# Kernel tuning notes

Measured on AMD Instinct MI355X. Metric: run time of the kernel, lower is better.

## Reference

```python
import jax, jax.numpy as jnp
import numpy as np

# config (matches init_kwargs)
NA, NEN = 8, 8            # n_agents, n_enemies
NENT = NA + NEN           # n_entities
NFA, NFE = 64, 64         # state_nf_al, state_nf_en
E, A, M, HE = 64, 64, 32, 64  # entity_embed, attn_embed, mixing_embed, hypernet_embed
TD, TE = 64, 64           # task_repre_dim, task_repre_embed_dim
BS, SL = 64, 512


def setup_inputs() -> dict:
    key = jax.random.key(0)
    ks = iter(jax.random.split(key, 32))
    def rn(shape, scale=0.05):
        return jax.random.normal(next(ks), shape, dtype=jnp.float32) * scale
    return {
        "agent_qs": rn((BS, SL, NA), 1.0),
        "states": rn((BS, SL, NA * NFA + NEN * NFE), 1.0),
        "task_repre_mu": rn((BS, SL, NA, TD), 1.0),
        "ally_w": rn((NFA, E)), "ally_b": rn((E,)),
        "enemy_w": rn((NFE, E)), "enemy_b": rn((E,)),
        "q_w": rn((E, A)), "q_b": rn((A,)),
        "k_w": rn((E, A)), "k_b": rn((A,)),
        "hw1_w1": rn((E + NFA + TE, HE)), "hw1_b1": rn((HE,)),
        "hw1_w2": rn((HE, M)), "hw1_b2": rn((M,)),
        "hwf_w1": rn((E + TE, HE)), "hwf_b1": rn((HE,)),
        "hwf_w2": rn((HE, M)), "hwf_b2": rn((M,)),
        "hb1_w": rn((E + TE, M)), "hb1_b": rn((M,)),
        "v_w1": rn((E + TE, M)), "v_b1": rn((M,)),
        "v_w2": rn((M, 1)), "v_b2": rn((1,)),
        "tre_w": rn((TD, TE)), "tre_b": rn((TE,)),
    }


def reference(agent_qs, states, task_repre_mu,
              ally_w, ally_b, enemy_w, enemy_b,
              q_w, q_b, k_w, k_b,
              hw1_w1, hw1_b1, hw1_w2, hw1_b2,
              hwf_w1, hwf_b1, hwf_w2, hwf_b2,
              hb1_w, hb1_b, v_w1, v_b1, v_w2, v_b2,
              tre_w, tre_b):
    bs, sl = agent_qs.shape[:2]
    # decompose_state (state_last_action=False, state_timestep_number=False)
    ally = states[..., : NA * NFA].reshape(bs, sl, NA, NFA)      # [bs,sl,NA,NFA]
    enemy = states[..., NA * NFA:].reshape(bs, sl, NEN, NFE)     # [bs,sl,NEN,NFE]
    ally_e = ally @ ally_w + ally_b                              # [bs,sl,NA,E]
    enemy_e = enemy @ enemy_w + enemy_b                          # [bs,sl,NEN,E]
    ent = jnp.concatenate([ally_e, enemy_e], axis=2)             # [bs,sl,NENT,E]
    q = ent @ q_w + q_b                                          # [bs,sl,NENT,A]
    k = ent @ k_w + k_b
    energy = jnp.einsum('bsqa,bska->bsqk', q, k)                 # [bs,sl,NENT,NENT]
    # torch: F.softmax(energy, dim=1) on [B,n_ent,n_ent] -> softmax over query axis
    attn = jax.nn.softmax(energy, axis=2)
    # attn_out = bmm(value[B,E,n], attn[B,n,n]).mean(-1)
    attn_out = jnp.einsum('bsne,bsnk->bse', ent, attn) / NENT    # [bs,sl,E]

    mean_mu = task_repre_mu.mean(axis=-2)                        # [bs,sl,TD]
    tre = task_repre_mu @ tre_w + tre_b                          # [bs,sl,NA,TE]
    mean_tre = mean_mu @ tre_w + tre_b                           # [bs,sl,TE]

    ent_mix = jnp.concatenate([
        jnp.broadcast_to(attn_out[:, :, None, :], (bs, sl, NA, E)),
        ally, tre], axis=-1)                                     # [bs,sl,NA,E+NFA+TE]
    mix = jnp.concatenate([attn_out, mean_tre], axis=-1)         # [bs,sl,E+TE]

    w1 = jnp.abs(jax.nn.relu(ent_mix @ hw1_w1 + hw1_b1) @ hw1_w2 + hw1_b2)  # [bs,sl,NA,M]
    b1 = mix @ hb1_w + hb1_b                                     # [bs,sl,M]
    hidden = jax.nn.elu(jnp.einsum('bsn,bsnm->bsm', agent_qs, w1) + b1)     # [bs,sl,M]
    wf = jnp.abs(jax.nn.relu(mix @ hwf_w1 + hwf_b1) @ hwf_w2 + hwf_b2)      # [bs,sl,M]
    v = jax.nn.relu(mix @ v_w1 + v_b1) @ v_w2 + v_b2             # [bs,sl,1]
    q_tot = jnp.einsum('bsm,bsm->bs', hidden, wf)[..., None] + v # [bs,sl,1]
    return q_tot
```

## Files before the change

### kernel.cpp

```cpp
#include <hip/hip_runtime.h>
#include <math.h>


#define TOKS 32768

typedef __attribute__((ext_vector_type(8))) short short8;
typedef __attribute__((ext_vector_type(4))) float f32x4;

#define MFMA(a, b, c) __builtin_amdgcn_mfma_f32_16x16x32_bf16((a), (b), (c), 0, 0, 0)

#define E_CAT   0
#define E_WQKT  8192
#define E_ZBRT  13312
#define E_H1T   29696
#define E_W2T   41984
#define E_WFT   44032
#define E_BF16_TOTAL 46080
#define E_AO_US 46464

__device__ __forceinline__ unsigned short bfr(float x) {
    unsigned u = __builtin_bit_cast(unsigned, x);
    u += 0x7fffu + ((u >> 16) & 1u);
    return (unsigned short)(u >> 16);
}
__device__ __forceinline__ float bf2f(unsigned short h) {
    unsigned u = ((unsigned)h) << 16;
    return __builtin_bit_cast(float, u);
}
__device__ __forceinline__ short8 cvt8v(float4 a, float4 b) {
    short8 r;
    r[0] = (short)bfr(a.x); r[1] = (short)bfr(a.y);
    r[2] = (short)bfr(a.z); r[3] = (short)bfr(a.w);
    r[4] = (short)bfr(b.x); r[5] = (short)bfr(b.y);
    r[6] = (short)bfr(b.z); r[7] = (short)bfr(b.w);
    return r;
}
#define SWZ64(r, c)  ((((r) * 64)  + (c)) ^ (((r) & 7) << 3))
#define SWZ128(r, c) ((((r) * 128) + (c)) ^ (((r) & 7) << 3))
#define SWZ192(r, c) ((((r) * 192) + (c)) ^ (((r) & 7) << 3))

__global__ __launch_bounds__(256) void qmix_setup(
    const float* __restrict__ ally_w, const float* __restrict__ enemy_w,
    const float* __restrict__ q_w, const float* __restrict__ k_w,
    const float* __restrict__ k_b,
    const float* __restrict__ hw1_w1, const float* __restrict__ hw1_b1,
    const float* __restrict__ hw1_w2,
    const float* __restrict__ hwf_w1, const float* __restrict__ hwf_b1,
    const float* __restrict__ hwf_w2,
    const float* __restrict__ hb1_w, const float* __restrict__ hb1_b,
    const float* __restrict__ v_w1, const float* __restrict__ v_b1,
    const float* __restrict__ tre_w, const float* __restrict__ tre_b,
    unsigned short* __restrict__ wsb, float* __restrict__ wsf)
{
    int gid = blockIdx.x * 256 + threadIdx.x;
    if (gid < E_BF16_TOTAL) {
        float v = 0.f;
        int base, r, c, K;
        if (gid < E_WQKT) {
            base = E_CAT; K = 128;
            int i = gid - base; r = i >> 7; c = i & 127;
            v = (c < 64) ? ally_w[c * 64 + r] : enemy_w[(c - 64) * 64 + r];
        } else if (gid < E_ZBRT) {
            base = E_WQKT; K = 64;
            int i = gid - base; r = i >> 6; c = i & 63;
            if (r < 64) {
                for (int g = 0; g < 64; ++g) v += q_w[c * 64 + g] * k_w[r * 64 + g];
            } else if (r == 64) {
                for (int g = 0; g < 64; ++g) v += q_w[c * 64 + g] * k_b[g];
            }
        } else if (gid < E_H1T) {
            base = E_ZBRT; K = 128;
            int i = gid - base; r = i >> 7; c = i & 127;
            if (r < 64) {
                if (c < 64) v = hwf_w1[c * 64 + r];
                else for (int g = 0; g < 64; ++g) v += tre_w[(c - 64) * 64 + g] * hwf_w1[(64 + g) * 64 + r];
            } else if (r < 96) {
                int m = r - 64;
                if (c < 64) v = hb1_w[c * 32 + m];
                else for (int g = 0; g < 64; ++g) v += tre_w[(c - 64) * 64 + g] * hb1_w[(64 + g) * 32 + m];
            } else {
                int m = r - 96;
                if (c < 64) v = v_w1[c * 32 + m];
                else for (int g = 0; g < 64; ++g) v += tre_w[(c - 64) * 64 + g] * v_w1[(64 + g) * 32 + m];
            }
        } else if (gid < E_W2T) {
            base = E_H1T; K = 192;
            int i = gid - base; r = i / 192; c = i % 192;
            if (c < 64) v = hw1_w1[(64 + c) * 64 + r];
            else if (c < 128) {
                for (int g = 0; g < 64; ++g) v += tre_w[(c - 64) * 64 + g] * hw1_w1[(128 + g) * 64 + r];
            } else v = hw1_w1[(c - 128) * 64 + r];
        } else if (gid < E_WFT) {
            base = E_W2T; K = 64;
            int i = gid - base; r = i >> 6; c = i & 63;
            v = hw1_w2[c * 32 + r];
        } else {
            base = E_WFT; K = 64;
            int i = gid - base; r = i >> 6; c = i & 63;
            v = hwf_w2[c * 32 + r];
        }
        wsb[base + ((r * K + c) ^ ((r & 7) << 3))] = bfr(v);
    } else if (gid < E_BF16_TOTAL + 192) {
        int j = gid - E_BF16_TOTAL; float v;
        if (j < 64) {
            v = hw1_b1[j];
            for (int g = 0; g < 64; ++g) v += tre_b[g] * hw1_w1[(128 + g) * 64 + j];
        } else if (j < 128) {
            int e = j - 64; v = hwf_b1[e];
            for (int g = 0; g < 64; ++g) v += tre_b[g] * hwf_w1[(64 + g) * 64 + e];
        } else if (j < 160) {
            int m = j - 128; v = hb1_b[m];
            for (int g = 0; g < 64; ++g) v += tre_b[g] * hb1_w[(64 + g) * 32 + m];
        } else {
            int m = j - 160; v = v_b1[m];
            for (int g = 0; g < 64; ++g) v += tre_b[g] * v_w1[(64 + g) * 32 + m];
        }
        wsf[j] = v;
    }
}

__global__ __launch_bounds__(512) void qmix_attn(
    const float* __restrict__ states,
    const float* __restrict__ ally_b, const float* __restrict__ enemy_b,
    const unsigned short* __restrict__ wsb,
    unsigned short* __restrict__ aoG)
{
    __shared__ unsigned short sWa[13312];
    __shared__ unsigned short sE[8][1024];
    __shared__ unsigned short sT[8][1024];

    const int lane = threadIdx.x & 63;
    const int wv   = threadIdx.x >> 6;
    const int l15  = lane & 15;
    const int lg   = lane >> 4;
    const int kb   = lg * 8;
    const int tok0 = blockIdx.x * 32;

    const short8 zero8 = {0, 0, 0, 0, 0, 0, 0, 0};
    const f32x4  zero4 = {0.f, 0.f, 0.f, 0.f};

    for (int i = threadIdx.x * 8; i < 13312; i += 512 * 8)
        *(short8*)(sWa + i) = *(const short8*)(wsb + E_CAT + i);
    __syncthreads();
    const unsigned short* lCAT  = sWa;
    const unsigned short* lWQKT = sWa + 8192;

    unsigned short* E = sE[wv];
    unsigned short* T = sT[wv];

    float biasEnt[4];
    #pragma unroll
    for (int nt = 0; nt < 4; ++nt) {
        int col = nt * 16 + l15;
        biasEnt[nt] = (lg < 2) ? ally_b[col] : enemy_b[col];
    }

    const int roff = (l15 < 8) ? (l15 * 64 + kb) : (512 + (l15 - 8) * 64 + kb);
    float4 pf[4];
    {
        const float* p = states + (size_t)(tok0 + wv * 4) * 1024 + roff;
        pf[0] = *(const float4*)(p);      pf[1] = *(const float4*)(p + 4);
        pf[2] = *(const float4*)(p + 32); pf[3] = *(const float4*)(p + 36);
    }

    for (int ti = 0; ti < 4; ++ti) {
        const size_t t = (size_t)(tok0 + wv * 4 + ti);
        float4 cur0 = pf[0], cur1 = pf[1], cur2 = pf[2], cur3 = pf[3];
        if (ti < 3) {
            const float* p = states + (t + 1) * 1024 + roff;
            pf[0] = *(const float4*)(p);      pf[1] = *(const float4*)(p + 4);
            pf[2] = *(const float4*)(p + 32); pf[3] = *(const float4*)(p + 36);
        }
        short8 a01 = cvt8v(cur0, cur1);
        short8 a23 = cvt8v(cur2, cur3);
        const bool isally = (l15 < 8);

        f32x4 accB[4] = {zero4, zero4, zero4, zero4};
        #pragma unroll
        for (int ks = 0; ks < 4; ++ks) {
            short8 af;
            if (ks == 0)      af = isally ? a01 : zero8;
            else if (ks == 1) af = isally ? a23 : zero8;
            else if (ks == 2) af = isally ? zero8 : a01;
            else              af = isally ? zero8 : a23;
            #pragma unroll
            for (int nt = 0; nt < 4; ++nt) {
                short8 w = *(const short8*)&lCAT[SWZ128(nt * 16 + l15, ks * 32 + kb)];
                accB[nt] = MFMA(af, w, accB[nt]);
            }
        }
        float entv[4][4];
        #pragma unroll
        for (int nt = 0; nt < 4; ++nt) {
            #pragma unroll
            for (int reg = 0; reg < 4; ++reg) {
                entv[nt][reg] = accB[nt][reg] + biasEnt[nt];
                E[SWZ64(lg * 4 + reg, nt * 16 + l15)] = bfr(entv[nt][reg]);
            }
        }

        f32x4 accC[5] = {zero4, zero4, zero4, zero4, zero4};
        #pragma unroll
        for (int ks = 0; ks < 2; ++ks) {
            short8 ef = *(const short8*)&E[SWZ64(l15, ks * 32 + kb)];
            #pragma unroll
            for (int nt = 0; nt < 5; ++nt) {
                short8 w = *(const short8*)&lWQKT[SWZ64(nt * 16 + l15, ks * 32 + kb)];
                accC[nt] = MFMA(ef, w, accC[nt]);
            }
        }
        const int src = lane & 48;
        float si[4];
        #pragma unroll
        for (int reg = 0; reg < 4; ++reg) si[reg] = __shfl(accC[4][reg], src);
        #pragma unroll
        for (int nt = 0; nt < 4; ++nt)
            #pragma unroll
            for (int reg = 0; reg < 4; ++reg)
                T[SWZ64(lg * 4 + reg, nt * 16 + l15)] = bfr(accC[nt][reg]);

        f32x4 en = zero4;
        #pragma unroll
        for (int ks = 0; ks < 2; ++ks) {
            short8 ta = *(const short8*)&T[SWZ64(l15, ks * 32 + kb)];
            short8 ba = *(const short8*)&E[SWZ64(l15, ks * 32 + kb)];
            en = MFMA(ta, ba, en);
        }
        #pragma unroll
        for (int reg = 0; reg < 4; ++reg) en[reg] += si[reg];

        float mx = fmaxf(fmaxf(en[0], en[1]), fmaxf(en[2], en[3]));
        mx = fmaxf(mx, __shfl_xor(mx, 16));
        mx = fmaxf(mx, __shfl_xor(mx, 32));
        float p0 = __expf(en[0] - mx), p1 = __expf(en[1] - mx);
        float p2 = __expf(en[2] - mx), p3 = __expf(en[3] - mx);
        float s = p0 + p1 + p2 + p3;
        s += __shfl_xor(s, 16);
        s += __shfl_xor(s, 32);
        float inv = 1.f / s;
        float r0 = p0 * inv, r1 = p1 * inv, r2 = p2 * inv, r3 = p3 * inv;
        r0 += __shfl_xor(r0, 1); r0 += __shfl_xor(r0, 2); r0 += __shfl_xor(r0, 4); r0 += __shfl_xor(r0, 8);
        r1 += __shfl_xor(r1, 1); r1 += __shfl_xor(r1, 2); r1 += __shfl_xor(r1, 4); r1 += __shfl_xor(r1, 8);
        r2 += __shfl_xor(r2, 1); r2 += __shfl_xor(r2, 2); r2 += __shfl_xor(r2, 4); r2 += __shfl_xor(r2, 8);
        r3 += __shfl_xor(r3, 1); r3 += __shfl_xor(r3, 2); r3 += __shfl_xor(r3, 4); r3 += __shfl_xor(r3, 8);

        float part[4];
        #pragma unroll
        for (int nt = 0; nt < 4; ++nt) {
            float pp = r0 * entv[nt][0] + r1 * entv[nt][1]
                     + r2 * entv[nt][2] + r3 * entv[nt][3];
            pp += __shfl_xor(pp, 16);
            pp += __shfl_xor(pp, 32);
            part[nt] = pp;
        }
        float ao = (lg == 0) ? part[0] : (lg == 1) ? part[1]
                 : (lg == 2) ? part[2] : part[3];
        aoG[t * 64 + lane] = bfr(ao * 0.0625f);
    }
}

__device__ __forceinline__ short8 mmfrag(const float* __restrict__ mp) {
    float a0 = 0.f, a1 = 0.f, a2 = 0.f, a3 = 0.f, a4 = 0.f, a5 = 0.f, a6 = 0.f, a7 = 0.f;
    #pragma unroll
    for (int a = 0; a < 8; ++a) {
        float4 u = *(const float4*)(mp + a * 64);
        float4 v = *(const float4*)(mp + a * 64 + 4);
        a0 += u.x; a1 += u.y; a2 += u.z; a3 += u.w;
        a4 += v.x; a5 += v.y; a6 += v.z; a7 += v.w;
    }
    return cvt8v(make_float4(a0 * 0.125f, a1 * 0.125f, a2 * 0.125f, a3 * 0.125f),
                 make_float4(a4 * 0.125f, a5 * 0.125f, a6 * 0.125f, a7 * 0.125f));
}

__global__ __launch_bounds__(256) void qmix_hyper(
    const float* __restrict__ agent_qs, const float* __restrict__ states,
    const float* __restrict__ mu,
    const float* __restrict__ v_w2, const float* __restrict__ v_b2,
    const float* __restrict__ hw1_b2, const float* __restrict__ hwf_b2,
    const unsigned short* __restrict__ wsb, const float* __restrict__ wsf,
    const unsigned short* __restrict__ aoG,
    float* __restrict__ out)
{
    __shared__ unsigned short sWb[16384];
    __shared__ unsigned short sZ[4][1024];
    __shared__ unsigned short sH1[4][2048];
    __shared__ float sB1[4][512];
    __shared__ float sWF[4][512];
    __shared__ float sV[4][16];

    const int lane = threadIdx.x & 63;
    const int wv   = threadIdx.x >> 6;
    const int l15  = lane & 15;
    const int lg   = lane >> 4;
    const int kb   = lg * 8;
    const int T0   = blockIdx.x * 64 + wv * 16;

    const float* BHF = wsf + 64;
    const float* BB1 = wsf + 128;
    const float* BV  = wsf + 160;
    const float* BH1 = wsf + 0;

    const f32x4 zero4 = {0.f, 0.f, 0.f, 0.f};

    for (int i = threadIdx.x * 8; i < 16384; i += 256 * 8)
        *(short8*)(sWb + i) = *(const short8*)(wsb + E_ZBRT + i);
    __syncthreads();

    f32x4 zb[8] = {zero4, zero4, zero4, zero4, zero4, zero4, zero4, zero4};
    #pragma unroll
    for (int ks = 0; ks < 4; ++ks) {
        short8 af;
        if (ks < 2)
            af = *(const short8*)&aoG[(size_t)(T0 + l15) * 64 + ks * 32 + kb];
        else
            af = mmfrag(mu + (size_t)(T0 + l15) * 512 + (ks - 2) * 32 + kb);
        #pragma unroll
        for (int nt = 0; nt < 8; ++nt) {
            short8 w = *(const short8*)&sWb[SWZ128(nt * 16 + l15, ks * 32 + kb)];
            zb[nt] = MFMA(af, w, zb[nt]);
        }
    }
    __syncthreads();

    for (int i = threadIdx.x * 8; i < 16384; i += 256 * 8)
        *(short8*)(sWb + i) = *(const short8*)(wsb + E_H1T + i);

    #pragma unroll
    for (int nt = 0; nt < 4; ++nt) {
        int col = nt * 16 + l15;
        float bz = BHF[col];
        #pragma unroll
        for (int reg = 0; reg < 4; ++reg)
            sZ[wv][SWZ64(lg * 4 + reg, col)] = bfr(fmaxf(zb[nt][reg] + bz, 0.f));
    }
    #pragma unroll
    for (int nt = 4; nt < 6; ++nt) {
        int m = (nt - 4) * 16 + l15;
        float bb = BB1[m];
        #pragma unroll
        for (int reg = 0; reg < 4; ++reg)
            sB1[wv][(lg * 4 + reg) * 32 + m] = zb[nt][reg] + bb;
    }
    {
        float bv0 = BV[l15], bv1 = BV[16 + l15];
        float vw0 = v_w2[l15], vw1 = v_w2[16 + l15];
        #pragma unroll
        for (int reg = 0; reg < 4; ++reg) {
            float vp = fmaxf(zb[6][reg] + bv0, 0.f) * vw0
                     + fmaxf(zb[7][reg] + bv1, 0.f) * vw1;
            vp += __shfl_xor(vp, 1); vp += __shfl_xor(vp, 2);
            vp += __shfl_xor(vp, 4); vp += __shfl_xor(vp, 8);
            if (l15 == 0) sV[wv][lg * 4 + reg] = vp;
        }
    }
    __syncthreads();
    const unsigned short* lH1T = sWb;
    const unsigned short* lW2T = sWb + 12288;
    const unsigned short* lWFT = sWb + 14336;

    {
        f32x4 wfa = zero4, wfb = zero4;
        #pragma unroll
        for (int ks = 0; ks < 2; ++ks) {
            short8 af = *(const short8*)&sZ[wv][SWZ64(l15, ks * 32 + kb)];
            short8 b0 = *(const short8*)&lWFT[SWZ64(l15, ks * 32 + kb)];
            short8 b1 = *(const short8*)&lWFT[SWZ64(16 + l15, ks * 32 + kb)];
            wfa = MFMA(af, b0, wfa);
            wfb = MFMA(af, b1, wfb);
        }
        float hb0 = hwf_b2[l15], hb1 = hwf_b2[16 + l15];
        #pragma unroll
        for (int reg = 0; reg < 4; ++reg) {
            int tok = lg * 4 + reg;
            sWF[wv][tok * 32 + l15]      = fabsf(wfa[reg] + hb0);
            sWF[wv][tok * 32 + 16 + l15] = fabsf(wfb[reg] + hb1);
        }
    }

    const float vb2 = v_b2[0];
    const float b20 = hw1_b2[l15], b21 = hw1_b2[16 + l15];
    const int agent = l15 & 7;

    for (int c = 0; c < 4; ++c) {
        f32x4 h[2][4] = {{zero4, zero4, zero4, zero4}, {zero4, zero4, zero4, zero4}};
        #pragma unroll
        for (int ks = 0; ks < 6; ++ks) {
            #pragma unroll
            for (int ff = 0; ff < 2; ++ff) {
                const size_t tok = (size_t)(T0 + c * 4 + ff * 2 + (l15 >> 3));
                short8 af;
                if (ks < 2)
                    af = cvt8v(*(const float4*)(states + tok * 1024 + agent * 64 + ks * 32 + kb),
                               *(const float4*)(states + tok * 1024 + agent * 64 + ks * 32 + kb + 4));
                else if (ks < 4)
                    af = cvt8v(*(const float4*)(mu + tok * 512 + agent * 64 + (ks - 2) * 32 + kb),
                               *(const float4*)(mu + tok * 512 + agent * 64 + (ks - 2) * 32 + kb + 4));
                else
                    af = *(const short8*)&aoG[tok * 64 + (ks - 4) * 32 + kb];
                #pragma unroll
                for (int nt = 0; nt < 4; ++nt) {
                    short8 w = *(const short8*)&lH1T[SWZ192(nt * 16 + l15, ks * 32 + kb)];
                    h[ff][nt] = MFMA(af, w, h[ff][nt]);
                }
            }
        }
        #pragma unroll
        for (int ff = 0; ff < 2; ++ff)
            #pragma unroll
            for (int nt = 0; nt < 4; ++nt) {
                int col = nt * 16 + l15;
                float bh = BH1[col];
                #pragma unroll
                for (int reg = 0; reg < 4; ++reg)
                    sH1[wv][SWZ64(ff * 16 + lg * 4 + reg, col)] =
                        bfr(fmaxf(h[ff][nt][reg] + bh, 0.f));
            }

        f32x4 wa[2] = {zero4, zero4}, wb[2] = {zero4, zero4};
        #pragma unroll
        for (int ks = 0; ks < 2; ++ks) {
            short8 b0 = *(const short8*)&lW2T[SWZ64(l15, ks * 32 + kb)];
            short8 b1 = *(const short8*)&lW2T[SWZ64(16 + l15, ks * 32 + kb)];
            #pragma unroll
            for (int ff = 0; ff < 2; ++ff) {
                short8 af = *(const short8*)&sH1[wv][SWZ64(ff * 16 + l15, ks * 32 + kb)];
                wa[ff] = MFMA(af, b0, wa[ff]);
                wb[ff] = MFMA(af, b1, wb[ff]);
            }
        }

        #pragma unroll
        for (int ff = 0; ff < 2; ++ff) {
            const int tokL = c * 4 + ff * 2 + (lg >> 1);
            float hp0 = 0.f, hp1 = 0.f;
            #pragma unroll
            for (int reg = 0; reg < 4; ++reg) {
                float qsv = agent_qs[(size_t)(T0 + tokL) * 8 + (lg & 1) * 4 + reg];
                hp0 += qsv * fabsf(wa[ff][reg] + b20);
                hp1 += qsv * fabsf(wb[ff][reg] + b21);
            }
            hp0 += __shfl_xor(hp0, 16);
            hp1 += __shfl_xor(hp1, 16);
            float e0 = hp0 + sB1[wv][tokL * 32 + l15];
            float e1 = hp1 + sB1[wv][tokL * 32 + 16 + l15];
            float hid0 = e0 > 0.f ? e0 : (__expf(e0) - 1.f);
            float hid1 = e1 > 0.f ? e1 : (__expf(e1) - 1.f);
            float q = hid0 * sWF[wv][tokL * 32 + l15]
                    + hid1 * sWF[wv][tokL * 32 + 16 + l15];
            q += __shfl_xor(q, 1); q += __shfl_xor(q, 2);
            q += __shfl_xor(q, 4); q += __shfl_xor(q, 8);
            if (l15 == 0 && (lg & 1) == 0)
                out[T0 + tokL] = q + sV[wv][tokL] + vb2;
        }
    }
}

extern "C" void kernel_launch(void* const* d_in, const int* in_sizes, int n_in,
                              void* d_out, int out_size, void* d_ws, size_t ws_size,
                              hipStream_t stream)
{
    const float* agent_qs = (const float*)d_in[0];
    const float* states   = (const float*)d_in[1];
    const float* mu       = (const float*)d_in[2];
    const float* ally_w   = (const float*)d_in[3];
    const float* ally_b   = (const float*)d_in[4];
    const float* enemy_w  = (const float*)d_in[5];
    const float* enemy_b  = (const float*)d_in[6];
    const float* q_w      = (const float*)d_in[7];
    const float* k_w      = (const float*)d_in[9];
    const float* k_b      = (const float*)d_in[10];
    const float* hw1_w1   = (const float*)d_in[11];
    const float* hw1_b1   = (const float*)d_in[12];
    const float* hw1_w2   = (const float*)d_in[13];
    const float* hw1_b2   = (const float*)d_in[14];
    const float* hwf_w1   = (const float*)d_in[15];
    const float* hwf_b1   = (const float*)d_in[16];
    const float* hwf_w2   = (const float*)d_in[17];
    const float* hwf_b2   = (const float*)d_in[18];
    const float* hb1_w    = (const float*)d_in[19];
    const float* hb1_b    = (const float*)d_in[20];
    const float* v_w1     = (const float*)d_in[21];
    const float* v_b1     = (const float*)d_in[22];
    const float* v_w2     = (const float*)d_in[23];
    const float* v_b2     = (const float*)d_in[24];
    const float* tre_w    = (const float*)d_in[25];
    const float* tre_b    = (const float*)d_in[26];

    unsigned short* wsb = (unsigned short*)d_ws;
    float* wsf = (float*)((char*)d_ws + (size_t)E_BF16_TOTAL * 2);
    unsigned short* aoG = wsb + E_AO_US;
    float* out = (float*)d_out;

    hipLaunchKernelGGL(qmix_setup, dim3(181), dim3(256), 0, stream,
                       ally_w, enemy_w, q_w, k_w, k_b,
                       hw1_w1, hw1_b1, hw1_w2,
                       hwf_w1, hwf_b1, hwf_w2,
                       hb1_w, hb1_b, v_w1, v_b1, tre_w, tre_b,
                       wsb, wsf);

    hipLaunchKernelGGL(qmix_attn, dim3(TOKS / 32), dim3(512), 0, stream,
                       states, ally_b, enemy_b, wsb, aoG);

    hipLaunchKernelGGL(qmix_hyper, dim3(TOKS / 64), dim3(256), 0, stream,
                       agent_qs, states, mu, v_w2, v_b2, hw1_b2, hwf_b2,
                       wsb, wsf, aoG, out);
}
```

Baseline: 95.25 us.

## Process one token per wave in attention kernel, issuing state loads before weight barrier

The attention kernel now gives each wave a single token instead of looping over four with software prefetch, so the grid grows fourfold. The state loads and bias loads are issued before the shared-memory weight staging barrier to overlap global latency with the weight copy. The cost is that every block reloads the 26 KB weight table into LDS for only 8 tokens, which multiplies LDS staging traffic and L2 reads by four.

```diff
diff --git a/kernel.cpp b/kernel.cpp
--- a/kernel.cpp
+++ b/kernel.cpp
@@ -134,13 +134,27 @@
     const int l15  = lane & 15;
     const int lg   = lane >> 4;
     const int kb   = lg * 8;
-    const int tok0 = blockIdx.x * 32;
+    const size_t t = (size_t)blockIdx.x * 8 + wv;
 
     const short8 zero8 = {0, 0, 0, 0, 0, 0, 0, 0};
     const f32x4  zero4 = {0.f, 0.f, 0.f, 0.f};
 
     for (int i = threadIdx.x * 8; i < 13312; i += 512 * 8)
         *(short8*)(sWa + i) = *(const short8*)(wsb + E_CAT + i);
+
+    const int roff = (l15 < 8) ? (l15 * 64 + kb) : (512 + (l15 - 8) * 64 + kb);
+    const float* p = states + t * 1024 + roff;
+    float4 cur0 = *(const float4*)(p);
+    float4 cur1 = *(const float4*)(p + 4);
+    float4 cur2 = *(const float4*)(p + 32);
+    float4 cur3 = *(const float4*)(p + 36);
+
+    float biasEnt[4];
+    #pragma unroll
+    for (int nt = 0; nt < 4; ++nt) {
+        int col = nt * 16 + l15;
+        biasEnt[nt] = (lg < 2) ? ally_b[col] : enemy_b[col];
+    }
     __syncthreads();
     const unsigned short* lCAT  = sWa;
     const unsigned short* lWQKT = sWa + 8192;
@@ -148,115 +162,91 @@
     unsigned short* E = sE[wv];
     unsigned short* T = sT[wv];
 
-    float biasEnt[4];
+    short8 a01 = cvt8v(cur0, cur1);
+    short8 a23 = cvt8v(cur2, cur3);
+    const bool isally = (l15 < 8);
+
+    f32x4 accB[4] = {zero4, zero4, zero4, zero4};
+    #pragma unroll
+    for (int ks = 0; ks < 4; ++ks) {
+        short8 af;
+        if (ks == 0)      af = isally ? a01 : zero8;
+        else if (ks == 1) af = isally ? a23 : zero8;
+        else if (ks == 2) af = isally ? zero8 : a01;
+        else              af = isally ? zero8 : a23;
+        #pragma unroll
+        for (int nt = 0; nt < 4; ++nt) {
+            short8 w = *(const short8*)&lCAT[SWZ128(nt * 16 + l15, ks * 32 + kb)];
+            accB[nt] = MFMA(af, w, accB[nt]);
+        }
+    }
+    float entv[4][4];
     #pragma unroll
     for (int nt = 0; nt < 4; ++nt) {
-        int col = nt * 16 + l15;
-        biasEnt[nt] = (lg < 2) ? ally_b[col] : enemy_b[col];
-    }
-
-    const int roff = (l15 < 8) ? (l15 * 64 + kb) : (512 + (l15 - 8) * 64 + kb);
-    float4 pf[4];
+        #pragma unroll
+        for (int reg = 0; reg < 4; ++reg) {
+            entv[nt][reg] = accB[nt][reg] + biasEnt[nt];
+            E[SWZ64(lg * 4 + reg, nt * 16 + l15)] = bfr(entv[nt][reg]);
+        }
+    }
+
+    f32x4 accC[5] = {zero4, zero4, zero4, zero4, zero4};
+    short8 ef0 = *(const short8*)&E[SWZ64(l15, 0 * 32 + kb)];
+    short8 ef1 = *(const short8*)&E[SWZ64(l15, 1 * 32 + kb)];
+    #pragma unroll
+    for (int nt = 0; nt < 5; ++nt) {
+        short8 w0 = *(const short8*)&lWQKT[SWZ64(nt * 16 + l15, 0 * 32 + kb)];
+        short8 w1 = *(const short8*)&lWQKT[SWZ64(nt * 16 + l15, 1 * 32 + kb)];
+        accC[nt] = MFMA(ef0, w0, accC[nt]);
+        accC[nt] = MFMA(ef1, w1, accC[nt]);
+    }
+    const int src = lane & 48;
+    float si[4];
+    #pragma unroll
+    for (int reg = 0; reg < 4; ++reg) si[reg] = __shfl(accC[4][reg], src);
+    #pragma unroll
+    for (int nt = 0; nt < 4; ++nt)
+        #pragma unroll
+        for (int reg = 0; reg < 4; ++reg)
+            T[SWZ64(lg * 4 + reg, nt * 16 + l15)] = bfr(accC[nt][reg]);
+
+    f32x4 en = zero4;
     {
-        const float* p = states + (size_t)(tok0 + wv * 4) * 1024 + roff;
-        pf[0] = *(const float4*)(p);      pf[1] = *(const float4*)(p + 4);
-        pf[2] = *(const float4*)(p + 32); pf[3] = *(const float4*)(p + 36);
-    }
-
-    for (int ti = 0; ti < 4; ++ti) {
-        const size_t t = (size_t)(tok0 + wv * 4 + ti);
-        float4 cur0 = pf[0], cur1 = pf[1], cur2 = pf[2], cur3 = pf[3];
-        if (ti < 3) {
-            const float* p = states + (t + 1) * 1024 + roff;
-            pf[0] = *(const float4*)(p);      pf[1] = *(const float4*)(p + 4);
-            pf[2] = *(const float4*)(p + 32); pf[3] = *(const float4*)(p + 36);
-        }
-        short8 a01 = cvt8v(cur0, cur1);
-        short8 a23 = cvt8v(cur2, cur3);
-        const bool isally = (l15 < 8);
-
-        f32x4 accB[4] = {zero4, zero4, zero4, zero4};
-        #pragma unroll
-        for (int ks = 0; ks < 4; ++ks) {
-            short8 af;
-            if (ks == 0)      af = isally ? a01 : zero8;
-            else if (ks == 1) af = isally ? a23 : zero8;
-            else if (ks == 2) af = isally ? zero8 : a01;
-            else              af = isally ? zero8 : a23;
-            #pragma unroll
-            for (int nt = 0; nt < 4; ++nt) {
-                short8 w = *(const short8*)&lCAT[SWZ128(nt * 16 + l15, ks * 32 + kb)];
-                accB[nt] = MFMA(af, w, accB[nt]);
-            }
-        }
-        float entv[4][4];
-        #pragma unroll
-        for (int nt = 0; nt < 4; ++nt) {
-            #pragma unroll
-            for (int reg = 0; reg < 4; ++reg) {
-                entv[nt][reg] = accB[nt][reg] + biasEnt[nt];
-                E[SWZ64(lg * 4 + reg, nt * 16 + l15)] = bfr(entv[nt][reg]);
-            }
-        }
-
-        f32x4 accC[5] = {zero4, zero4, zero4, zero4, zero4};
-        #pragma unroll
-        for (int ks = 0; ks < 2; ++ks) {
-            short8 ef = *(const short8*)&E[SWZ64(l15, ks * 32 + kb)];
-            #pragma unroll
-            for (int nt = 0; nt < 5; ++nt) {
-                short8 w = *(const short8*)&lWQKT[SWZ64(nt * 16 + l15, ks * 32 + kb)];
-                accC[nt] = MFMA(ef, w, accC[nt]);
-            }
-        }
-        const int src = lane & 48;
-        float si[4];
-        #pragma unroll
-        for (int reg = 0; reg < 4; ++reg) si[reg] = __shfl(accC[4][reg], src);
-        #pragma unroll
-        for (int nt = 0; nt < 4; ++nt)
-            #pragma unroll
-            for (int reg = 0; reg < 4; ++reg)
-                T[SWZ64(lg * 4 + reg, nt * 16 + l15)] = bfr(accC[nt][reg]);
-
-        f32x4 en = zero4;
-        #pragma unroll
-        for (int ks = 0; ks < 2; ++ks) {
-            short8 ta = *(const short8*)&T[SWZ64(l15, ks * 32 + kb)];
-            short8 ba = *(const short8*)&E[SWZ64(l15, ks * 32 + kb)];
-            en = MFMA(ta, ba, en);
-        }
-        #pragma unroll
-        for (int reg = 0; reg < 4; ++reg) en[reg] += si[reg];
-
-        float mx = fmaxf(fmaxf(en[0], en[1]), fmaxf(en[2], en[3]));
-        mx = fmaxf(mx, __shfl_xor(mx, 16));
-        mx = fmaxf(mx, __shfl_xor(mx, 32));
-        float p0 = __expf(en[0] - mx), p1 = __expf(en[1] - mx);
-        float p2 = __expf(en[2] - mx), p3 = __expf(en[3] - mx);
-        float s = p0 + p1 + p2 + p3;
-        s += __shfl_xor(s, 16);
-        s += __shfl_xor(s, 32);
-        float inv = 1.f / s;
-        float r0 = p0 * inv, r1 = p1 * inv, r2 = p2 * inv, r3 = p3 * inv;
-        r0 += __shfl_xor(r0, 1); r0 += __shfl_xor(r0, 2); r0 += __shfl_xor(r0, 4); r0 += __shfl_xor(r0, 8);
-        r1 += __shfl_xor(r1, 1); r1 += __shfl_xor(r1, 2); r1 += __shfl_xor(r1, 4); r1 += __shfl_xor(r1, 8);
-        r2 += __shfl_xor(r2, 1); r2 += __shfl_xor(r2, 2); r2 += __shfl_xor(r2, 4); r2 += __shfl_xor(r2, 8);
-        r3 += __shfl_xor(r3, 1); r3 += __shfl_xor(r3, 2); r3 += __shfl_xor(r3, 4); r3 += __shfl_xor(r3, 8);
-
-        float part[4];
-        #pragma unroll
-        for (int nt = 0; nt < 4; ++nt) {
-            float pp = r0 * entv[nt][0] + r1 * entv[nt][1]
-                     + r2 * entv[nt][2] + r3 * entv[nt][3];
-            pp += __shfl_xor(pp, 16);
-            pp += __shfl_xor(pp, 32);
-            part[nt] = pp;
-        }
-        float ao = (lg == 0) ? part[0] : (lg == 1) ? part[1]
-                 : (lg == 2) ? part[2] : part[3];
-        aoG[t * 64 + lane] = bfr(ao * 0.0625f);
-    }
+        short8 ta0 = *(const short8*)&T[SWZ64(l15, 0 * 32 + kb)];
+        short8 ta1 = *(const short8*)&T[SWZ64(l15, 1 * 32 + kb)];
+        en = MFMA(ta0, ef0, en);
+        en = MFMA(ta1, ef1, en);
+    }
+    #pragma unroll
+    for (int reg = 0; reg < 4; ++reg) en[reg] += si[reg];
+
+    float mx = fmaxf(fmaxf(en[0], en[1]), fmaxf(en[2], en[3]));
+    mx = fmaxf(mx, __shfl_xor(mx, 16));
+    mx = fmaxf(mx, __shfl_xor(mx, 32));
+    float p0 = __expf(en[0] - mx), p1 = __expf(en[1] - mx);
+    float p2 = __expf(en[2] - mx), p3 = __expf(en[3] - mx);
+    float s = p0 + p1 + p2 + p3;
+    s += __shfl_xor(s, 16);
+    s += __shfl_xor(s, 32);
+    float inv = 1.f / s;
+    float r0 = p0 * inv, r1 = p1 * inv, r2 = p2 * inv, r3 = p3 * inv;
+    r0 += __shfl_xor(r0, 1); r0 += __shfl_xor(r0, 2); r0 += __shfl_xor(r0, 4); r0 += __shfl_xor(r0, 8);
+    r1 += __shfl_xor(r1, 1); r1 += __shfl_xor(r1, 2); r1 += __shfl_xor(r1, 4); r1 += __shfl_xor(r1, 8);
+    r2 += __shfl_xor(r2, 1); r2 += __shfl_xor(r2, 2); r2 += __shfl_xor(r2, 4); r2 += __shfl_xor(r2, 8);
+    r3 += __shfl_xor(r3, 1); r3 += __shfl_xor(r3, 2); r3 += __shfl_xor(r3, 4); r3 += __shfl_xor(r3, 8);
+
+    float part[4];
+    #pragma unroll
+    for (int nt = 0; nt < 4; ++nt) {
+        float pp = r0 * entv[nt][0] + r1 * entv[nt][1]
+                 + r2 * entv[nt][2] + r3 * entv[nt][3];
+        pp += __shfl_xor(pp, 16);
+        pp += __shfl_xor(pp, 32);
+        part[nt] = pp;
+    }
+    float ao = (lg == 0) ? part[0] : (lg == 1) ? part[1]
+             : (lg == 2) ? part[2] : part[3];
+    aoG[t * 64 + lane] = bfr(ao * 0.0625f);
 }
 
 __device__ __forceinline__ short8 mmfrag(const float* __restrict__ mp) {
@@ -498,7 +488,7 @@
                        hb1_w, hb1_b, v_w1, v_b1, tre_w, tre_b,
                        wsb, wsf);
 
-    hipLaunchKernelGGL(qmix_attn, dim3(TOKS / 32), dim3(512), 0, stream,
+    hipLaunchKernelGGL(qmix_attn, dim3(TOKS / 8), dim3(512), 0, stream,
                        states, ally_b, enemy_b, wsb, aoG);
 
     hipLaunchKernelGGL(qmix_hyper, dim3(TOKS / 64), dim3(256), 0, stream,
```

After: 91.36 us. 4.1% less time.
